# Optimization experiments

Hardware: AMD Instinct MI355X
Metric: run time of the kernel (lower is better)

The kernel has to match this reference:

```python
import jax, jax.numpy as jnp
import numpy as np

N_NODES = 100000  # static segment count for segment_sum
DEGREE = 2        # polynomial degree of the Laplacian filter


def setup_inputs() -> dict:
    key = jax.random.key(0)
    k1, k2, k3, k4 = jax.random.split(key, 4)
    N, E, C = N_NODES, 1600000, 32
    x = jax.random.normal(k1, (N, C), dtype=jnp.float32)
    weights = jax.random.normal(k2, (1 + DEGREE,), dtype=jnp.float32)
    edge_src = jax.random.randint(k3, (E,), 0, N, dtype=jnp.int32)
    edge_dst = jax.random.randint(k4, (E,), 0, N, dtype=jnp.int32)
    return {"x": x, "weights": weights, "edge_src": edge_src, "edge_dst": edge_dst}


def reference(x, weights, edge_src, edge_dst):
    """y = (w0 * I + w1 * L + ... + w_d * L^d) @ x with L = D - A,
    computed by the recurrence t_k = L @ t_{k-1} (never materializing L^k)."""
    N = N_NODES
    # node degrees: D[i] = number of edges landing on i
    deg = jax.ops.segment_sum(jnp.ones_like(edge_src, dtype=x.dtype), edge_dst,
                              num_segments=N)  # [N]

    def lap_matvec(t):
        # (L @ t)[i] = deg[i] * t[i] - sum_{(s->i) in E} t[s]
        agg = jax.ops.segment_sum(t[edge_src], edge_dst, num_segments=N)  # [N, C]
        return deg[:, None] * t - agg

    y = weights[0] * x
    t = x
    for k in range(1, 1 + DEGREE):  # fixed small loop over polynomial order
        t = lap_matvec(t)
        y = y + weights[k] * t
    return y
```

## Files before the change

### kernel.cpp

```cpp
#include <hip/hip_runtime.h>

#define C 32
#define NT 256
#define BSH 8
#define BNODE 256
#define CAPC 5632
#define SRCMASK 0x1FFFF

typedef float f32x4 __attribute__((ext_vector_type(4)));

__device__ __forceinline__ unsigned int f2bf(float f) {
    unsigned int u = __float_as_uint(f);
    return (u + 0x7FFFu + ((u >> 16) & 1u)) >> 16;
}
__device__ __forceinline__ float bflo(unsigned int u) { return __uint_as_float(u << 16); }
__device__ __forceinline__ float bfhi(unsigned int u) { return __uint_as_float(u & 0xFFFF0000u); }

__global__ __launch_bounds__(1024) void phaseA_cvt(const int* __restrict__ src,
                                                   const int* __restrict__ dst,
                                                   int* __restrict__ cursor,
                                                   int* __restrict__ pk,
                                                   const float* __restrict__ x,
                                                   uint2* __restrict__ xb2,
                                                   int N, int E, int nbuck, int chunk) {
    extern __shared__ int l[];
    int* lcnt = l;
    int* lcur = l + nbuck;
    int tid = threadIdx.x;
    for (int i = tid; i < nbuck; i += 1024) lcnt[i] = 0;
    __syncthreads();
    int base = blockIdx.x * chunk;
    int end  = min(base + chunk, E);
    for (int e = base + tid; e < end; e += 1024)
        atomicAdd(&lcnt[dst[e] >> BSH], 1);
    __syncthreads();
    for (int i = tid; i < nbuck; i += 1024) {
        int c = lcnt[i];
        lcur[i] = i * CAPC + (c ? atomicAdd(&cursor[i], c) : 0);
    }
    __syncthreads();
    for (int e = base + tid; e < end; e += 1024) {
        int d = dst[e];
        int b = d >> BSH;
        int pos = atomicAdd(&lcur[b], 1);
        pk[pos] = src[e] | ((d & (BNODE - 1)) << 17);
    }
    int total = N * 8;
    int gid = blockIdx.x * 1024 + tid;
    int gth = gridDim.x * 1024;
    for (int i = gid; i < total; i += gth) {
        f32x4 v = *(const f32x4*)(x + (size_t)i * 4);
        uint2 r;
        r.x = f2bf(v.x) | (f2bf(v.y) << 16);
        r.y = f2bf(v.z) | (f2bf(v.w) << 16);
        xb2[i] = r;
    }
}

__device__ __forceinline__ void accum_lds(const uint2* __restrict__ arr,
                                          const int* idx,
                                          int lo, int hi, int lq,
                                          float& a0, float& a1, float& a2, float& a3) {
#define ACC4(u) { a0 += bflo(u.x); a1 += bfhi(u.x); a2 += bflo(u.y); a3 += bfhi(u.y); }
    int j = lo;
    for (; j + 7 < hi; j += 8) {
        int s0 = idx[j],     s1 = idx[j + 1], s2 = idx[j + 2], s3 = idx[j + 3];
        int s4 = idx[j + 4], s5 = idx[j + 5], s6 = idx[j + 6], s7 = idx[j + 7];
        uint2 u0 = arr[(size_t)s0 * 8 + lq];
        uint2 u1 = arr[(size_t)s1 * 8 + lq];
        uint2 u2 = arr[(size_t)s2 * 8 + lq];
        uint2 u3 = arr[(size_t)s3 * 8 + lq];
        uint2 u4 = arr[(size_t)s4 * 8 + lq];
        uint2 u5 = arr[(size_t)s5 * 8 + lq];
        uint2 u6 = arr[(size_t)s6 * 8 + lq];
        uint2 u7 = arr[(size_t)s7 * 8 + lq];
        ACC4(u0) ACC4(u1) ACC4(u2) ACC4(u3) ACC4(u4) ACC4(u5) ACC4(u6) ACC4(u7)
    }
    for (; j + 3 < hi; j += 4) {
        int s0 = idx[j], s1 = idx[j + 1], s2 = idx[j + 2], s3 = idx[j + 3];
        uint2 u0 = arr[(size_t)s0 * 8 + lq];
        uint2 u1 = arr[(size_t)s1 * 8 + lq];
        uint2 u2 = arr[(size_t)s2 * 8 + lq];
        uint2 u3 = arr[(size_t)s3 * 8 + lq];
        ACC4(u0) ACC4(u1) ACC4(u2) ACC4(u3)
    }
    for (; j < hi; ++j) {
        uint2 u0 = arr[(size_t)idx[j] * 8 + lq];
        ACC4(u0)
    }
#undef ACC4
}

__global__ __launch_bounds__(1024) void phaseB_mv1(int* __restrict__ pk,
                                                   const int* __restrict__ cursor,
                                                   int* __restrict__ row_start,
                                                   int* __restrict__ ideg,
                                                   const uint2* __restrict__ xb2,
                                                   uint2* __restrict__ t1b2, int N) {
    __shared__ int ent[CAPC];
    __shared__ int sorted[CAPC];
    __shared__ int h[BNODE];
    __shared__ int ss[BNODE];
    __shared__ int cur[BNODE];
    int b = blockIdx.x;
    int tid = threadIdx.x;
    int n0 = b << BSH;
    int base = b * CAPC;
    int cnt = min(cursor[b], CAPC);

    if (tid < BNODE) h[tid] = 0;
    __syncthreads();
    for (int i = tid; i < cnt; i += 1024) {
        int en = __builtin_nontemporal_load(&pk[base + i]);
        ent[i] = en;
        atomicAdd(&h[en >> 17], 1);
    }
    __syncthreads();
    int v = 0;
    if (tid < BNODE) { v = h[tid]; ss[tid] = v; }
    __syncthreads();
    for (int off = 1; off < BNODE; off <<= 1) {
        int u = 0;
        if (tid < BNODE && tid >= off) u = ss[tid - off];
        __syncthreads();
        if (tid < BNODE) ss[tid] += u;
        __syncthreads();
    }
    if (tid < BNODE) {
        int exc = ss[tid] - v;
        int n = n0 + tid;
        if (n < N) { row_start[n] = base + exc; ideg[n] = v; }
        cur[tid] = exc;
    }
    __syncthreads();
    for (int i = tid; i < cnt; i += 1024) {
        int en = ent[i];
        int pos = atomicAdd(&cur[en >> 17], 1);
        int s = en & SRCMASK;
        sorted[pos] = s;
        pk[base + pos] = s;
    }
    __syncthreads();

    for (int it = tid; it < BNODE * 8; it += 1024) {
        int r = it >> 3;
        int lq = it & 7;
        int n = n0 + r;
        if (n >= N) continue;
        int hi = ss[r];
        int lo = hi - h[r];
        float a0 = 0.f, a1 = 0.f, a2 = 0.f, a3 = 0.f;
        accum_lds(xb2, sorted, lo, hi, lq, a0, a1, a2, a3);
        uint2 xs = xb2[(size_t)n * 8 + lq];
        float fdg = (float)h[r];
        uint2 rr;
        rr.x = f2bf(fdg * bflo(xs.x) - a0) | (f2bf(fdg * bfhi(xs.x) - a1) << 16);
        rr.y = f2bf(fdg * bflo(xs.y) - a2) | (f2bf(fdg * bfhi(xs.y) - a3) << 16);
        t1b2[(size_t)n * 8 + lq] = rr;
    }
}

__global__ __launch_bounds__(1024) void gather2_lds(const uint2* __restrict__ xb2,
        const uint2* __restrict__ t1b2, const int* __restrict__ pk,
        const int* __restrict__ cursor, const int* __restrict__ row_start,
        const int* __restrict__ ideg, const float* __restrict__ wts,
        float* __restrict__ y, int N) {
    __shared__ int stg[CAPC];
    int b = blockIdx.x;
    int tid = threadIdx.x;
    int n0 = b << BSH;
    int base = b * CAPC;
    int cnt = min(cursor[b], CAPC);
    for (int i = tid; i < cnt; i += 1024)
        stg[i] = __builtin_nontemporal_load(&pk[base + i]);
    __syncthreads();
    float w0 = wts[0], w1 = wts[1], w2 = wts[2];
    for (int it = tid; it < BNODE * 8; it += 1024) {
        int r = it >> 3;
        int lq = it & 7;
        int n = n0 + r;
        if (n >= N) continue;
        int dg = ideg[n];
        int lo = row_start[n] - base;
        int hi = lo + dg;
        float a0 = 0.f, a1 = 0.f, a2 = 0.f, a3 = 0.f;
        accum_lds(t1b2, stg, lo, hi, lq, a0, a1, a2, a3);
        uint2 xs = xb2[(size_t)n * 8 + lq];
        uint2 ts = t1b2[(size_t)n * 8 + lq];
        float fdg = (float)dg;
        f32x4 rq;
        rq.x = w0 * bflo(xs.x) + w1 * bflo(ts.x) + w2 * (fdg * bflo(ts.x) - a0);
        rq.y = w0 * bfhi(xs.x) + w1 * bfhi(ts.x) + w2 * (fdg * bfhi(ts.x) - a1);
        rq.z = w0 * bflo(xs.y) + w1 * bflo(ts.y) + w2 * (fdg * bflo(ts.y) - a2);
        rq.w = w0 * bfhi(xs.y) + w1 * bfhi(ts.y) + w2 * (fdg * bfhi(ts.y) - a3);
        __builtin_nontemporal_store(rq, (f32x4*)(y + (size_t)n * C + lq * 4));
    }
}

extern "C" void kernel_launch(void* const* d_in, const int* in_sizes, int n_in,
                              void* d_out, int out_size, void* d_ws, size_t ws_size,
                              hipStream_t stream) {
    const float* x    = (const float*)d_in[0];
    const float* wts  = (const float*)d_in[1];
    const int*   esrc = (const int*)d_in[2];
    const int*   edst = (const int*)d_in[3];
    float*       y    = (float*)d_out;

    const int N = in_sizes[0] / C;
    const int E = in_sizes[2];
    const int nbuck = (N + BNODE - 1) >> BSH;
    const int nc = N * C;

    char* p = (char*)d_ws;
    auto align16 = [](size_t s) { return (s + 15) & ~(size_t)15; };
    int* cursor    = (int*)p; p += align16((size_t)nbuck * 4);
    int* row_start = (int*)p; p += align16((size_t)N * 4);
    int* ideg      = (int*)p; p += align16((size_t)N * 4);
    int* pk        = (int*)p; p += align16((size_t)nbuck * CAPC * 4);
    uint2* xb2     = (uint2*)p; p += align16((size_t)nc * 2);
    uint2* t1b2    = (uint2*)p; p += align16((size_t)nc * 2);
    (void)ws_size;

    hipMemsetAsync(cursor, 0, (size_t)nbuck * 4, stream);

    const int ABLK = 512;
    const int chunk = (E + ABLK - 1) / ABLK;
    const size_t lds_a = (size_t)nbuck * 2 * 4;

    phaseA_cvt<<<ABLK, 1024, lds_a, stream>>>(esrc, edst, cursor, pk, x, xb2,
                                              N, E, nbuck, chunk);
    phaseB_mv1<<<nbuck, 1024, 0, stream>>>(pk, cursor, row_start, ideg,
                                           xb2, t1b2, N);
    gather2_lds<<<nbuck, 1024, 0, stream>>>(xb2, t1b2, pk, cursor, row_start,
                                            ideg, wts, y, N);
}
```

Before: 164.1 us.

## Split bf16 feature tables into two channel halves to shrink gather working set

The bf16 copies of x and t1 are stored as two separate half-tables of 16 channels each (32 bytes per node), and both gather kernels now process one half at a time. Each pass therefore gathers from a table half the size, which is meant to make random neighbour reads hit in cache more often. The cost is that every edge list is traversed twice and each gathered element is a 4-byte load instead of 8 bytes. The sorted source indices are also written back to global memory in a separate coalesced pass rather than scattered during the sort.

```diff
diff --git a/kernel.cpp b/kernel.cpp
--- a/kernel.cpp
+++ b/kernel.cpp
@@ -1,13 +1,13 @@
 #include <hip/hip_runtime.h>
 
 #define C 32
-#define NT 256
 #define BSH 8
 #define BNODE 256
 #define CAPC 5632
 #define SRCMASK 0x1FFFF
 
 typedef float f32x4 __attribute__((ext_vector_type(4)));
+typedef float f32x2 __attribute__((ext_vector_type(2)));
 
 __device__ __forceinline__ unsigned int f2bf(float f) {
     unsigned int u = __float_as_uint(f);
@@ -21,7 +21,7 @@
                                                    int* __restrict__ cursor,
                                                    int* __restrict__ pk,
                                                    const float* __restrict__ x,
-                                                   uint2* __restrict__ xb2,
+                                                   unsigned int* __restrict__ xbh,
                                                    int N, int E, int nbuck, int chunk) {
     extern __shared__ int l[];
     int* lcnt = l;
@@ -53,50 +53,52 @@
         uint2 r;
         r.x = f2bf(v.x) | (f2bf(v.y) << 16);
         r.y = f2bf(v.z) | (f2bf(v.w) << 16);
-        xb2[i] = r;
-    }
-}
-
-__device__ __forceinline__ void accum_lds(const uint2* __restrict__ arr,
-                                          const int* idx,
-                                          int lo, int hi, int lq,
-                                          float& a0, float& a1, float& a2, float& a3) {
-#define ACC4(u) { a0 += bflo(u.x); a1 += bfhi(u.x); a2 += bflo(u.y); a3 += bfhi(u.y); }
+        int node = i >> 3;
+        int q = i & 7;
+        int half = q >> 2;
+        ((uint2*)xbh)[((size_t)half * N + node) * 4 + (q & 3)] = r;
+    }
+}
+
+__device__ __forceinline__ void accum_h(const unsigned int* __restrict__ tab,
+                                        const int* idx, int lo, int hi, int lq,
+                                        float& a0, float& a1) {
+#define ACC2(u) { a0 += bflo(u); a1 += bfhi(u); }
     int j = lo;
     for (; j + 7 < hi; j += 8) {
         int s0 = idx[j],     s1 = idx[j + 1], s2 = idx[j + 2], s3 = idx[j + 3];
         int s4 = idx[j + 4], s5 = idx[j + 5], s6 = idx[j + 6], s7 = idx[j + 7];
-        uint2 u0 = arr[(size_t)s0 * 8 + lq];
-        uint2 u1 = arr[(size_t)s1 * 8 + lq];
-        uint2 u2 = arr[(size_t)s2 * 8 + lq];
-        uint2 u3 = arr[(size_t)s3 * 8 + lq];
-        uint2 u4 = arr[(size_t)s4 * 8 + lq];
-        uint2 u5 = arr[(size_t)s5 * 8 + lq];
-        uint2 u6 = arr[(size_t)s6 * 8 + lq];
-        uint2 u7 = arr[(size_t)s7 * 8 + lq];
-        ACC4(u0) ACC4(u1) ACC4(u2) ACC4(u3) ACC4(u4) ACC4(u5) ACC4(u6) ACC4(u7)
+        unsigned int u0 = tab[(size_t)s0 * 8 + lq];
+        unsigned int u1 = tab[(size_t)s1 * 8 + lq];
+        unsigned int u2 = tab[(size_t)s2 * 8 + lq];
+        unsigned int u3 = tab[(size_t)s3 * 8 + lq];
+        unsigned int u4 = tab[(size_t)s4 * 8 + lq];
+        unsigned int u5 = tab[(size_t)s5 * 8 + lq];
+        unsigned int u6 = tab[(size_t)s6 * 8 + lq];
+        unsigned int u7 = tab[(size_t)s7 * 8 + lq];
+        ACC2(u0) ACC2(u1) ACC2(u2) ACC2(u3) ACC2(u4) ACC2(u5) ACC2(u6) ACC2(u7)
     }
     for (; j + 3 < hi; j += 4) {
         int s0 = idx[j], s1 = idx[j + 1], s2 = idx[j + 2], s3 = idx[j + 3];
-        uint2 u0 = arr[(size_t)s0 * 8 + lq];
-        uint2 u1 = arr[(size_t)s1 * 8 + lq];
-        uint2 u2 = arr[(size_t)s2 * 8 + lq];
-        uint2 u3 = arr[(size_t)s3 * 8 + lq];
-        ACC4(u0) ACC4(u1) ACC4(u2) ACC4(u3)
+        unsigned int u0 = tab[(size_t)s0 * 8 + lq];
+        unsigned int u1 = tab[(size_t)s1 * 8 + lq];
+        unsigned int u2 = tab[(size_t)s2 * 8 + lq];
+        unsigned int u3 = tab[(size_t)s3 * 8 + lq];
+        ACC2(u0) ACC2(u1) ACC2(u2) ACC2(u3)
     }
     for (; j < hi; ++j) {
-        uint2 u0 = arr[(size_t)idx[j] * 8 + lq];
-        ACC4(u0)
-    }
-#undef ACC4
+        unsigned int u0 = tab[(size_t)idx[j] * 8 + lq];
+        ACC2(u0)
+    }
+#undef ACC2
 }
 
 __global__ __launch_bounds__(1024) void phaseB_mv1(int* __restrict__ pk,
                                                    const int* __restrict__ cursor,
                                                    int* __restrict__ row_start,
                                                    int* __restrict__ ideg,
-                                                   const uint2* __restrict__ xb2,
-                                                   uint2* __restrict__ t1b2, int N) {
+                                                   const unsigned int* __restrict__ xbh,
+                                                   unsigned int* __restrict__ t1h, int N) {
     __shared__ int ent[CAPC];
     __shared__ int sorted[CAPC];
     __shared__ int h[BNODE];
@@ -136,32 +138,35 @@
     for (int i = tid; i < cnt; i += 1024) {
         int en = ent[i];
         int pos = atomicAdd(&cur[en >> 17], 1);
-        int s = en & SRCMASK;
-        sorted[pos] = s;
-        pk[base + pos] = s;
-    }
-    __syncthreads();
-
-    for (int it = tid; it < BNODE * 8; it += 1024) {
-        int r = it >> 3;
-        int lq = it & 7;
-        int n = n0 + r;
-        if (n >= N) continue;
-        int hi = ss[r];
-        int lo = hi - h[r];
-        float a0 = 0.f, a1 = 0.f, a2 = 0.f, a3 = 0.f;
-        accum_lds(xb2, sorted, lo, hi, lq, a0, a1, a2, a3);
-        uint2 xs = xb2[(size_t)n * 8 + lq];
-        float fdg = (float)h[r];
-        uint2 rr;
-        rr.x = f2bf(fdg * bflo(xs.x) - a0) | (f2bf(fdg * bfhi(xs.x) - a1) << 16);
-        rr.y = f2bf(fdg * bflo(xs.y) - a2) | (f2bf(fdg * bfhi(xs.y) - a3) << 16);
-        t1b2[(size_t)n * 8 + lq] = rr;
-    }
-}
-
-__global__ __launch_bounds__(1024) void gather2_lds(const uint2* __restrict__ xb2,
-        const uint2* __restrict__ t1b2, const int* __restrict__ pk,
+        sorted[pos] = en & SRCMASK;
+    }
+    __syncthreads();
+    for (int i = tid; i < cnt; i += 1024)
+        pk[base + i] = sorted[i];
+
+    for (int hf = 0; hf < 2; ++hf) {
+        const unsigned int* tab = xbh + (size_t)hf * N * 8;
+        unsigned int* ttab = t1h + (size_t)hf * N * 8;
+        for (int it = tid; it < BNODE * 8; it += 1024) {
+            int r = it >> 3;
+            int lq = it & 7;
+            int n = n0 + r;
+            if (n >= N) continue;
+            int hi = ss[r];
+            int lo = hi - h[r];
+            float a0 = 0.f, a1 = 0.f;
+            accum_h(tab, sorted, lo, hi, lq, a0, a1);
+            unsigned int xs = tab[(size_t)n * 8 + lq];
+            float fdg = (float)h[r];
+            unsigned int rr = f2bf(fdg * bflo(xs) - a0)
+                            | (f2bf(fdg * bfhi(xs) - a1) << 16);
+            ttab[(size_t)n * 8 + lq] = rr;
+        }
+    }
+}
+
+__global__ __launch_bounds__(1024) void gather2_lds(const unsigned int* __restrict__ xbh,
+        const unsigned int* __restrict__ t1h, const int* __restrict__ pk,
         const int* __restrict__ cursor, const int* __restrict__ row_start,
         const int* __restrict__ ideg, const float* __restrict__ wts,
         float* __restrict__ y, int N) {
@@ -175,25 +180,28 @@
         stg[i] = __builtin_nontemporal_load(&pk[base + i]);
     __syncthreads();
     float w0 = wts[0], w1 = wts[1], w2 = wts[2];
-    for (int it = tid; it < BNODE * 8; it += 1024) {
-        int r = it >> 3;
-        int lq = it & 7;
-        int n = n0 + r;
-        if (n >= N) continue;
-        int dg = ideg[n];
-        int lo = row_start[n] - base;
-        int hi = lo + dg;
-        float a0 = 0.f, a1 = 0.f, a2 = 0.f, a3 = 0.f;
-        accum_lds(t1b2, stg, lo, hi, lq, a0, a1, a2, a3);
-        uint2 xs = xb2[(size_t)n * 8 + lq];
-        uint2 ts = t1b2[(size_t)n * 8 + lq];
-        float fdg = (float)dg;
-        f32x4 rq;
-        rq.x = w0 * bflo(xs.x) + w1 * bflo(ts.x) + w2 * (fdg * bflo(ts.x) - a0);
-        rq.y = w0 * bfhi(xs.x) + w1 * bfhi(ts.x) + w2 * (fdg * bfhi(ts.x) - a1);
-        rq.z = w0 * bflo(xs.y) + w1 * bflo(ts.y) + w2 * (fdg * bflo(ts.y) - a2);
-        rq.w = w0 * bfhi(xs.y) + w1 * bfhi(ts.y) + w2 * (fdg * bfhi(ts.y) - a3);
-        __builtin_nontemporal_store(rq, (f32x4*)(y + (size_t)n * C + lq * 4));
+    for (int hf = 0; hf < 2; ++hf) {
+        const unsigned int* xtab = xbh + (size_t)hf * N * 8;
+        const unsigned int* ttab = t1h + (size_t)hf * N * 8;
+        for (int it = tid; it < BNODE * 8; it += 1024) {
+            int r = it >> 3;
+            int lq = it & 7;
+            int n = n0 + r;
+            if (n >= N) continue;
+            int dg = ideg[n];
+            int lo = row_start[n] - base;
+            int hi = lo + dg;
+            float a0 = 0.f, a1 = 0.f;
+            accum_h(ttab, stg, lo, hi, lq, a0, a1);
+            unsigned int xs = xtab[(size_t)n * 8 + lq];
+            unsigned int ts = ttab[(size_t)n * 8 + lq];
+            float fdg = (float)dg;
+            f32x2 yv;
+            yv.x = w0 * bflo(xs) + w1 * bflo(ts) + w2 * (fdg * bflo(ts) - a0);
+            yv.y = w0 * bfhi(xs) + w1 * bfhi(ts) + w2 * (fdg * bfhi(ts) - a1);
+            __builtin_nontemporal_store(yv,
+                (f32x2*)(y + (size_t)n * C + hf * 16 + lq * 2));
+        }
     }
 }
 
@@ -217,20 +225,20 @@
     int* row_start = (int*)p; p += align16((size_t)N * 4);
     int* ideg      = (int*)p; p += align16((size_t)N * 4);
     int* pk        = (int*)p; p += align16((size_t)nbuck * CAPC * 4);
-    uint2* xb2     = (uint2*)p; p += align16((size_t)nc * 2);
-    uint2* t1b2    = (uint2*)p; p += align16((size_t)nc * 2);
+    unsigned int* xbh = (unsigned int*)p; p += align16((size_t)nc * 2);
+    unsigned int* t1h = (unsigned int*)p; p += align16((size_t)nc * 2);
     (void)ws_size;
 
-    hipMemsetAsync(cursor, 0, (size_t)nbuck * 4, stream);
+    (void)hipMemsetAsync(cursor, 0, (size_t)nbuck * 4, stream);
 
     const int ABLK = 512;
     const int chunk = (E + ABLK - 1) / ABLK;
     const size_t lds_a = (size_t)nbuck * 2 * 4;
 
-    phaseA_cvt<<<ABLK, 1024, lds_a, stream>>>(esrc, edst, cursor, pk, x, xb2,
+    phaseA_cvt<<<ABLK, 1024, lds_a, stream>>>(esrc, edst, cursor, pk, x, xbh,
                                               N, E, nbuck, chunk);
     phaseB_mv1<<<nbuck, 1024, 0, stream>>>(pk, cursor, row_start, ideg,
-                                           xb2, t1b2, N);
-    gather2_lds<<<nbuck, 1024, 0, stream>>>(xb2, t1b2, pk, cursor, row_start,
+                                           xbh, t1h, N);
+    gather2_lds<<<nbuck, 1024, 0, stream>>>(xbh, t1h, pk, cursor, row_start,
                                             ideg, wts, y, N);
 }
```

New measurement: 159.9 us. 1.03x faster.
